# Performance work log

Measured on AMD Instinct MI355X. Metric: run time of the kernel, lower is better.

## Reference

```python
import jax, jax.numpy as jnp
import numpy as np

D_MODEL = 2048
NUM_Q_HEADS = 32
NUM_KV_HEADS = 8
HEAD_DIM = D_MODEL // NUM_Q_HEADS  # 64
NUM_GROUPS = NUM_Q_HEADS // NUM_KV_HEADS  # 4


def setup_inputs() -> dict:
    key = jax.random.key(0)
    ks = jax.random.split(key, 9)
    s = 1.0 / np.sqrt(D_MODEL)
    x = jax.random.normal(ks[0], (2, 2048, D_MODEL), dtype=jnp.float32)
    Wq = jax.random.uniform(ks[1], (D_MODEL, NUM_Q_HEADS * HEAD_DIM), jnp.float32, -s, s)
    bq = jax.random.uniform(ks[2], (NUM_Q_HEADS * HEAD_DIM,), jnp.float32, -s, s)
    Wk = jax.random.uniform(ks[3], (D_MODEL, NUM_KV_HEADS * HEAD_DIM), jnp.float32, -s, s)
    bk = jax.random.uniform(ks[4], (NUM_KV_HEADS * HEAD_DIM,), jnp.float32, -s, s)
    Wv = jax.random.uniform(ks[5], (D_MODEL, NUM_KV_HEADS * HEAD_DIM), jnp.float32, -s, s)
    bv = jax.random.uniform(ks[6], (NUM_KV_HEADS * HEAD_DIM,), jnp.float32, -s, s)
    Wo = jax.random.uniform(ks[7], (D_MODEL, D_MODEL), jnp.float32, -s, s)
    bo = jax.random.uniform(ks[8], (D_MODEL,), jnp.float32, -s, s)
    return {"x": x, "Wq": Wq, "bq": bq, "Wk": Wk, "bk": bk,
            "Wv": Wv, "bv": bv, "Wo": Wo, "bo": bo}


def reference(x, Wq, bq, Wk, bk, Wv, bv, Wo, bo):
    B, T, C = x.shape
    Hkv, G, Dh = NUM_KV_HEADS, NUM_GROUPS, HEAD_DIM
    # projections
    q = (x @ Wq + bq).reshape(B, T, Hkv, G, Dh)   # group G query heads per kv head
    k = (x @ Wk + bk).reshape(B, T, Hkv, Dh)
    v = (x @ Wv + bv).reshape(B, T, Hkv, Dh)
    scale = 1.0 / np.sqrt(Dh).astype(np.float32)
    # scores: [B, Hkv, G, T, T] (kv head broadcast over its G query heads)
    scores = jnp.einsum('btkgd,bskd->bkgts', q, k) * scale
    attn = jax.nn.softmax(scores, axis=-1)
    out = jnp.einsum('bkgts,bskd->btkgd', attn, v).reshape(B, T, C)
    return out @ Wo + bo
```

## Files before the change

### kernel.cpp

```cpp
#include <hip/hip_runtime.h>
#include <cstdint>
#include <cstddef>
#include <math.h>

typedef uint16_t bf16;
typedef __attribute__((ext_vector_type(8))) __bf16 bf16x8;
typedef __attribute__((ext_vector_type(4))) float f32x4;
typedef __attribute__((ext_vector_type(16))) float f32x16;

#define MFMA16(a,b,c) __builtin_amdgcn_mfma_f32_16x16x32_bf16((a),(b),(c),0,0,0)
#define MFMA32(a,b,c) __builtin_amdgcn_mfma_f32_32x32x16_bf16((a),(b),(c),0,0,0)

__device__ __forceinline__ uint16_t f2bf(float f){
  uint32_t u = __float_as_uint(f);
  return (uint16_t)((u + 0x7fffu + ((u >> 16) & 1u)) >> 16);
}
__device__ __forceinline__ uint32_t pk2(float lo, float hi){
  return (uint32_t)f2bf(lo) | ((uint32_t)f2bf(hi) << 16);
}

__device__ __forceinline__ void gload_lds16(const void* g, void* l){
  __builtin_amdgcn_global_load_lds((const __attribute__((address_space(1))) void*)g,
                                   (__attribute__((address_space(3))) void*)l, 16, 0, 0);
}

__device__ __forceinline__ void transpose64(const float* __restrict__ in, bf16* __restrict__ out,
                                            int R, int C, int c0, int r0, float* tileRaw){
  float (*tile)[65] = reinterpret_cast<float(*)[65]>(tileRaw);
  int t = threadIdx.x;
  int fx = t & 15, fy = t >> 4;
  #pragma unroll
  for (int i = 0; i < 4; i++){
    int r = fy + i*16;
    float4 v = *reinterpret_cast<const float4*>(in + (size_t)(r0 + r)*C + c0 + fx*4);
    tile[r][fx*4+0] = v.x; tile[r][fx*4+1] = v.y;
    tile[r][fx*4+2] = v.z; tile[r][fx*4+3] = v.w;
  }
  __syncthreads();
  int gx = t & 7, gy = t >> 3;
  #pragma unroll
  for (int i = 0; i < 2; i++){
    int c = gy + i*32;
    int rr = gx*8;
    union { bf16 h[8]; uint4 u; } pk_;
    #pragma unroll
    for (int j = 0; j < 8; j++) pk_.h[j] = f2bf(tile[rr+j][c]);
    *reinterpret_cast<uint4*>(out + (size_t)(c0 + c)*R + r0 + rr) = pk_.u;
  }
}

__global__ void k_prep(const float* __restrict__ x, bf16* __restrict__ xb,
                       const float* __restrict__ Wq, bf16* __restrict__ WqT,
                       const float* __restrict__ Wk, bf16* __restrict__ WkT,
                       const float* __restrict__ Wv, bf16* __restrict__ WvT,
                       const float* __restrict__ Wo, bf16* __restrict__ WoT,
                       const float* __restrict__ bq, const float* __restrict__ bk,
                       const float* __restrict__ bv, float* __restrict__ biasAll){
  __shared__ __align__(16) float tile[64*65];
  int b = blockIdx.x;
  if (b < 8192){
    int i = (b * 256 + threadIdx.x) * 4;
    float4 v = *reinterpret_cast<const float4*>(x + i);
    uint2 pkv = make_uint2(pk2(v.x, v.y), pk2(v.z, v.w));
    *reinterpret_cast<uint2*>(xb + i) = pkv;
  } else if (b < 9216){
    int idx = b - 8192;
    transpose64(Wq, WqT, 2048, 2048, (idx & 31)*64, (idx >> 5)*64, tile);
  } else if (b < 9472){
    int idx = b - 9216;
    transpose64(Wk, WkT, 2048, 512, (idx & 7)*64, (idx >> 3)*64, tile);
  } else if (b < 9728){
    int idx = b - 9472;
    transpose64(Wv, WvT, 2048, 512, (idx & 7)*64, (idx >> 3)*64, tile);
  } else if (b < 10752){
    int idx = b - 9728;
    transpose64(Wo, WoT, 2048, 2048, (idx & 31)*64, (idx >> 5)*64, tile);
  } else {
    int j = (b - 10752)*1024 + threadIdx.x*4;
    float4 v;
    if (j < 2048)      v = *reinterpret_cast<const float4*>(bq + j);
    else if (j < 2560) v = *reinterpret_cast<const float4*>(bk + j - 2048);
    else               v = *reinterpret_cast<const float4*>(bv + j - 2560);
    *reinterpret_cast<float4*>(biasAll + j) = v;
  }
}

__device__ __forceinline__ void gemm256x192_core(
    const bf16* __restrict__ Abase, const bf16* __restrict__ Btbase,
    char* lds, f32x4 acc[8][3])
{
  const int tid = threadIdx.x;
  const int wid = tid >> 6, lane = tid & 63;
  const int wm = wid >> 2, wn = wid & 3;
  const int lr = lane & 15, lg = lane >> 4;
  const f32x4 vzero = {0.f, 0.f, 0.f, 0.f};
  #pragma unroll
  for (int m = 0; m < 8; m++)
    #pragma unroll
    for (int n = 0; n < 3; n++)
      acc[m][n] = vzero;

  int srcA[4], srcB[3];
  #pragma unroll
  for (int i = 0; i < 4; i++){
    int db = i*8192 + tid*16;
    int row = db >> 7, sp = (db >> 4) & 7, sl = sp ^ (row & 7);
    srcA[i] = row*2048 + sl*8;
  }
  #pragma unroll
  for (int i = 0; i < 3; i++){
    int db = i*8192 + tid*16;
    int row = db >> 7, sp = (db >> 4) & 7, sl = sp ^ (row & 7);
    srcB[i] = row*2048 + sl*8;
  }
  const int dOf = wid*1024;

  int ksl[2];
  #pragma unroll
  for (int ks = 0; ks < 2; ks++) ksl[ks] = (((ks*4 + lg) ^ (lr & 7)) << 4);
  const int aB = wm*16384 + lr*128;
  const int bB = wn*6144 + lr*128;

  #define STG_A(bufOff, koff) do { \
    gload_lds16(Abase + (koff) + srcA[0], lds + (bufOff) + dOf); \
    gload_lds16(Abase + (koff) + srcA[1], lds + (bufOff) + 8192 + dOf); \
    gload_lds16(Abase + (koff) + srcA[2], lds + (bufOff) + 16384 + dOf); \
    gload_lds16(Abase + (koff) + srcA[3], lds + (bufOff) + 24576 + dOf); \
  } while(0)
  #define STG_B(bufOff, koff) do { \
    gload_lds16(Btbase + (koff) + srcB[0], lds + (bufOff) + dOf); \
    gload_lds16(Btbase + (koff) + srcB[1], lds + (bufOff) + 8192 + dOf); \
    gload_lds16(Btbase + (koff) + srcB[2], lds + (bufOff) + 16384 + dOf); \
  } while(0)

  STG_B(98304, 0);
  STG_A(0, 0);
  STG_A(32768, 64);
  asm volatile("s_waitcnt vmcnt(4)" ::: "memory");
  __builtin_amdgcn_s_barrier();

  int aOff = 0;
  int bOff = 98304;
  for (int t = 0; t < 32; t++){
    const int aStg = (aOff == 0) ? 65536 : aOff - 32768;
    const int bNxt = bOff ^ 24576;

    if (t < 31) STG_B(bNxt, (t+1)*64);
    if (t < 30) STG_A(aStg, (t+2)*64);

    bf16x8 afr[8][2], bfr[3][2];
    #pragma unroll
    for (int am = 0; am < 8; am++)
      #pragma unroll
      for (int ks = 0; ks < 2; ks++)
        afr[am][ks] = *reinterpret_cast<const bf16x8*>(lds + aOff + aB + am*2048 + ksl[ks]);
    #pragma unroll
    for (int bn = 0; bn < 3; bn++)
      #pragma unroll
      for (int ks = 0; ks < 2; ks++)
        bfr[bn][ks] = *reinterpret_cast<const bf16x8*>(lds + bOff + bB + bn*2048 + ksl[ks]);

    __builtin_amdgcn_s_setprio(1);
    #pragma unroll
    for (int am = 0; am < 8; am++)
      #pragma unroll
      for (int bn = 0; bn < 3; bn++)
        #pragma unroll
        for (int ks = 0; ks < 2; ks++)
          acc[am][bn] = MFMA16(afr[am][ks], bfr[bn][ks], acc[am][bn]);
    __builtin_amdgcn_s_setprio(0);

    if (t < 30)       asm volatile("s_waitcnt vmcnt(4)" ::: "memory");
    else if (t == 30) asm volatile("s_waitcnt vmcnt(0)" ::: "memory");
    __builtin_amdgcn_s_barrier();

    aOff = (aOff == 65536) ? 0 : aOff + 32768;
    bOff = bNxt;
  }
  #undef STG_A
  #undef STG_B
}

__device__ __forceinline__ void gemm256x128_core(
    const bf16* __restrict__ Abase, const bf16* __restrict__ Btbase,
    char* lds, f32x4 acc[4][4])
{
  const int tid = threadIdx.x;
  const int wid = tid >> 6, lane = tid & 63;
  const int wm = wid >> 1, wn = wid & 1;
  const int lr = lane & 15, lg = lane >> 4;
  const f32x4 vzero = {0.f, 0.f, 0.f, 0.f};
  #pragma unroll
  for (int m = 0; m < 4; m++)
    #pragma unroll
    for (int n = 0; n < 4; n++)
      acc[m][n] = vzero;

  int srcA[4], srcB[2];
  #pragma unroll
  for (int i = 0; i < 4; i++){
    int db = i*8192 + tid*16;
    int row = db >> 7, sp = (db >> 4) & 7, sl = sp ^ (row & 7);
    srcA[i] = row*2048 + sl*8;
  }
  #pragma unroll
  for (int i = 0; i < 2; i++){
    int db = i*8192 + tid*16;
    int row = db >> 7, sp = (db >> 4) & 7, sl = sp ^ (row & 7);
    srcB[i] = row*2048 + sl*8;
  }
  const int dOf = wid*1024;

  int ksl[2];
  #pragma unroll
  for (int ks = 0; ks < 2; ks++) ksl[ks] = (((ks*4 + lg) ^ (lr & 7)) << 4);
  const int aB = wm*8192 + lr*128;
  const int bB = wn*8192 + lr*128;

  #define STG_A(bufOff, koff) do { \
    gload_lds16(Abase + (koff) + srcA[0], lds + (bufOff) + dOf); \
    gload_lds16(Abase + (koff) + srcA[1], lds + (bufOff) + 8192 + dOf); \
    gload_lds16(Abase + (koff) + srcA[2], lds + (bufOff) + 16384 + dOf); \
    gload_lds16(Abase + (koff) + srcA[3], lds + (bufOff) + 24576 + dOf); \
  } while(0)
  #define STG_B(bufOff, koff) do { \
    gload_lds16(Btbase + (koff) + srcB[0], lds + (bufOff) + dOf); \
    gload_lds16(Btbase + (koff) + srcB[1], lds + (bufOff) + 8192 + dOf); \
  } while(0)

  STG_B(98304, 0);
  STG_A(0, 0);
  STG_B(114688, 64);
  STG_A(32768, 64);
  asm volatile("s_waitcnt vmcnt(6)" ::: "memory");
  __builtin_amdgcn_s_barrier();

  int aOff = 0;
  int bIdx = 0;
  for (int t = 0; t < 32; t++){
    const int bOff = 98304 + bIdx*16384;
    const int aStg = (aOff == 0) ? 65536 : aOff - 32768;
    const int bStg = 98304 + ((bIdx == 0) ? 2 : bIdx - 1)*16384;

    if (t < 30){
      STG_B(bStg, (t+2)*64);
      STG_A(aStg, (t+2)*64);
    }

    bf16x8 afr[4][2], bfr[4][2];
    #pragma unroll
    for (int am = 0; am < 4; am++)
      #pragma unroll
      for (int ks = 0; ks < 2; ks++)
        afr[am][ks] = *reinterpret_cast<const bf16x8*>(lds + aOff + aB + am*2048 + ksl[ks]);
    #pragma unroll
    for (int bn = 0; bn < 4; bn++)
      #pragma unroll
      for (int ks = 0; ks < 2; ks++)
        bfr[bn][ks] = *reinterpret_cast<const bf16x8*>(lds + bOff + bB + bn*2048 + ksl[ks]);

    __builtin_amdgcn_s_setprio(1);
    #pragma unroll
    for (int am = 0; am < 4; am++)
      #pragma unroll
      for (int bn = 0; bn < 4; bn++)
        #pragma unroll
        for (int ks = 0; ks < 2; ks++)
          acc[am][bn] = MFMA16(afr[am][ks], bfr[bn][ks], acc[am][bn]);
    __builtin_amdgcn_s_setprio(0);

    if (t < 30)       asm volatile("s_waitcnt vmcnt(6)" ::: "memory");
    else if (t == 30) asm volatile("s_waitcnt vmcnt(0)" ::: "memory");
    __builtin_amdgcn_s_barrier();

    aOff = (aOff == 65536) ? 0 : aOff + 32768;
    bIdx = (bIdx == 2) ? 0 : bIdx + 1;
  }
  #undef STG_A
  #undef STG_B
}

__global__ __launch_bounds__(512, 1) void k_qkv(
    const bf16* __restrict__ xb, const bf16* __restrict__ WT,
    const float* __restrict__ biasAll,
    bf16* __restrict__ qo, bf16* __restrict__ ko, bf16* __restrict__ vtp)
{
  __shared__ __align__(16) char lds[147456];
  int m0 = blockIdx.x * 256;
  int y  = blockIdx.y;
  f32x4 acc[8][3];
  gemm256x192_core(xb + (size_t)m0*2048, WT + (size_t)y*192*2048, lds, acc);
  const int tid = threadIdx.x, wid = tid >> 6, lane = tid & 63;
  const int wm = wid >> 2, wn = wid & 3, lr = lane & 15, lg = lane >> 4;
  #pragma unroll
  for (int bn = 0; bn < 3; bn++){
    int fb = y*192 + wn*48 + bn*16;
    float bb = biasAll[fb + lr];
    if (fb < 2048){
      #pragma unroll
      for (int am = 0; am < 8; am++)
        #pragma unroll
        for (int r = 0; r < 4; r++){
          int row = m0 + wm*128 + am*16 + lg*4 + r;
          qo[(size_t)row*2048 + fb + lr] = f2bf((acc[am][bn][r] + bb) * 0.18033688011112042f);
        }
    } else if (fb < 2560){
      int c = fb - 2048 + lr;
      #pragma unroll
      for (int am = 0; am < 8; am++)
        #pragma unroll
        for (int r = 0; r < 4; r++){
          int row = m0 + wm*128 + am*16 + lg*4 + r;
          ko[(size_t)row*512 + c] = f2bf(acc[am][bn][r] + bb);
        }
    } else {
      int vcol = fb - 2560 + lr;
      #pragma unroll
      for (int am = 0; am < 8; am++){
        int row0 = m0 + wm*128 + am*16 + lg*4;
        int bi = row0 >> 11, tl = row0 & 2047;
        union { bf16 h[4]; uint2 u; } pk_;
        #pragma unroll
        for (int r = 0; r < 4; r++) pk_.h[r] = f2bf(acc[am][bn][r] + bb);
        *reinterpret_cast<uint2*>(vtp + ((size_t)bi*512 + vcol)*2048 + tl) = pk_.u;
      }
    }
  }
}

__global__ __launch_bounds__(512, 1) void k_oproj(
    const bf16* __restrict__ ab, const bf16* __restrict__ WoT,
    const float* __restrict__ bo, float* __restrict__ outp)
{
  __shared__ __align__(16) char lds[147456];
  int m0 = blockIdx.x * 256, n0 = blockIdx.y * 128;
  f32x4 acc[4][4];
  gemm256x128_core(ab + (size_t)m0*2048, WoT + (size_t)n0*2048, lds, acc);
  const int tid = threadIdx.x, wid = tid >> 6, lane = tid & 63;
  const int wm = wid >> 1, wn = wid & 1, lr = lane & 15, lg = lane >> 4;
  #pragma unroll
  for (int bn = 0; bn < 4; bn++){
    int col = n0 + wn*64 + bn*16 + lr;
    float bb = bo[col];
    #pragma unroll
    for (int am = 0; am < 4; am++)
      #pragma unroll
      for (int r = 0; r < 4; r++){
        int row = m0 + wm*64 + am*16 + lg*4 + r;
        outp[(size_t)row*2048 + col] = acc[am][bn][r] + bb;
      }
  }
}

__global__ __launch_bounds__(512, 2) void k_flash(
    const bf16* __restrict__ q, const bf16* __restrict__ kmat,
    const bf16* __restrict__ vt, bf16* __restrict__ ao)
{
  __shared__ __align__(16) char lds[98304];
  const int tid = threadIdx.x;
  const int wid = tid >> 6, lane = tid & 63;
  const int l31 = lane & 31, hi = lane >> 5;
  const int bh = blockIdx.y;
  const int b = bh >> 5, hq = bh & 31, kvh = hq >> 2;
  const int qt = blockIdx.x;
  const int qrow0 = b*2048 + qt*512 + wid*64;

  bf16x8 qf[2][4];
  #pragma unroll
  for (int g = 0; g < 2; g++){
    const bf16* qrow = q + (size_t)(qrow0 + g*32 + l31)*2048 + hq*64 + hi*8;
    #pragma unroll
    for (int t = 0; t < 4; t++)
      qf[g][t] = *reinterpret_cast<const bf16x8*>(qrow + t*16);
  }

  f32x16 oacc[2][2];
  #pragma unroll
  for (int g = 0; g < 2; g++)
    #pragma unroll
    for (int n = 0; n < 2; n++)
      #pragma unroll
      for (int r = 0; r < 16; r++) oacc[g][n][r] = 0.f;
  float rsg[2][2];
  rsg[0][0]=0.f; rsg[0][1]=0.f; rsg[1][0]=0.f; rsg[1][1]=0.f;
  const f32x16 zv = {0.f,0.f,0.f,0.f,0.f,0.f,0.f,0.f,0.f,0.f,0.f,0.f,0.f,0.f,0.f,0.f};

  const int r7 = l31 & 7;
  int A[4];
  #pragma unroll
  for (int j = 0; j < 4; j++)
    A[j] = l31*128 + (((2*j + hi) ^ r7) << 4);

  const bf16* kbase = kmat + (size_t)b*2048*512 + kvh*64;
  const bf16* vbase = vt + ((size_t)b*512 + kvh*64)*2048;

  int kSrc[2], vSrc[2];
  const int dOf = wid*1024;
  #pragma unroll
  for (int i = 0; i < 2; i++){
    int kdb = i*8192 + tid*16;
    int krow = kdb >> 7, ksp = (kdb >> 4) & 7, ksl = ksp ^ (krow & 7);
    kSrc[i] = krow*512 + ksl*8;
    int o = tid*16;
    int vrow = o >> 7, vsp = (o >> 4) & 7, vsl = vsp ^ (vrow & 7);
    vSrc[i] = vrow*2048 + i*64 + vsl*8;
  }

  #define STAGE(bo, st_) do { \
    const bf16* kb_ = kbase + (size_t)(st_)*128*512; \
    const bf16* vb_ = vbase + (st_)*128; \
    gload_lds16(kb_ + kSrc[0], lds + (bo) + dOf); \
    gload_lds16(kb_ + kSrc[1], lds + (bo) + 8192 + dOf); \
    gload_lds16(vb_ + vSrc[0], lds + 49152 + (bo) + dOf); \
    gload_lds16(vb_ + vSrc[1], lds + 49152 + (bo) + 8192 + dOf); \
  } while(0)

  #define LDK(j, imm) (*reinterpret_cast<const bf16x8*>(lds + kOff + A[j] + (imm)))
  #define LDV(j, imm) (*reinterpret_cast<const bf16x8*>(lds + 49152 + kOff + A[j] + (imm)))

  STAGE(0, 0);
  STAGE(16384, 1);

  int kOff = 0;
  int sOff = 32768;
  for (int st = 0; st < 16; st++){
    if (st == 15) asm volatile("s_waitcnt vmcnt(0)" ::: "memory");
    else          asm volatile("s_waitcnt vmcnt(4)" ::: "memory");
    __builtin_amdgcn_sched_barrier(0);
    __builtin_amdgcn_s_barrier();
    __builtin_amdgcn_sched_barrier(0);
    if (st < 14){
      STAGE(sOff, st+2);
      sOff = (sOff == 32768) ? 0 : sOff + 16384;
    }

    #pragma unroll
    for (int c = 0; c < 2; c++){
      f32x16 sc[2][2];
      __builtin_amdgcn_s_setprio(1);
      #pragma unroll
      for (int t = 0; t < 4; t++){
        bf16x8 af0 = LDK(t, c*8192);
        bf16x8 af1 = LDK(t, c*8192 + 4096);
        if (t == 0){
          sc[0][0] = MFMA32(af0, qf[0][0], zv);
          sc[1][0] = MFMA32(af0, qf[1][0], zv);
          sc[0][1] = MFMA32(af1, qf[0][0], zv);
          sc[1][1] = MFMA32(af1, qf[1][0], zv);
        } else {
          sc[0][0] = MFMA32(af0, qf[0][t], sc[0][0]);
          sc[1][0] = MFMA32(af0, qf[1][t], sc[1][0]);
          sc[0][1] = MFMA32(af1, qf[0][t], sc[0][1]);
          sc[1][1] = MFMA32(af1, qf[1][t], sc[1][1]);
        }
      }
      __builtin_amdgcn_s_setprio(0);

      uint32_t pw[2][2][8];
      #pragma unroll
      for (int g = 0; g < 2; g++){
        #pragma unroll
        for (int n = 0; n < 2; n++)
          #pragma unroll
          for (int j = 0; j < 8; j++){
            float plo = __builtin_amdgcn_exp2f(sc[g][n][2*j]);
            float phi = __builtin_amdgcn_exp2f(sc[g][n][2*j+1]);
            rsg[g][j & 1] += plo + phi;
            asm("v_cvt_pk_bf16_f32 %0, %1, %2" : "=v"(pw[g][n][j]) : "v"(plo), "v"(phi));
          }
        #pragma unroll
        for (int n = 0; n < 2; n++)
          #pragma unroll
          for (int h = 0; h < 2; h++){
            asm volatile("v_permlane32_swap_b32 %0, %1" : "+v"(pw[g][n][h*4+0]), "+v"(pw[g][n][h*4+2]));
            asm volatile("v_permlane32_swap_b32 %0, %1" : "+v"(pw[g][n][h*4+1]), "+v"(pw[g][n][h*4+3]));
          }
      }

      __builtin_amdgcn_s_setprio(1);
      #pragma unroll
      for (int kk = 0; kk < 4; kk++){
        int n = kk >> 1, h = kk & 1;
        union { uint32_t w[4]; bf16x8 v; } pa0, pa1;
        #pragma unroll
        for (int w_ = 0; w_ < 4; w_++){ pa0.w[w_] = pw[0][n][h*4+w_]; pa1.w[w_] = pw[1][n][h*4+w_]; }
        #pragma unroll
        for (int nd = 0; nd < 2; nd++){
          bf16x8 vf = LDV(kk, c*8192 + nd*4096);
          oacc[0][nd] = MFMA32(pa0.v, vf, oacc[0][nd]);
          oacc[1][nd] = MFMA32(pa1.v, vf, oacc[1][nd]);
        }
      }
      __builtin_amdgcn_s_setprio(0);
    }
    kOff = (kOff == 32768) ? 0 : kOff + 16384;
  }
  #undef STAGE
  #undef LDK
  #undef LDV

  #pragma unroll
  for (int g = 0; g < 2; g++){
    float rs = rsg[g][0] + rsg[g][1];
    float l = rs + __shfl_xor(rs, 32);
    float linv = 1.f / l;
    float lv[16];
    #pragma unroll
    for (int r = 0; r < 16; r++){
      int qi = (r & 3) + 8*(r >> 2) + 4*hi;
      lv[r] = __shfl(linv, qi);
    }
    #pragma unroll
    for (int nd = 0; nd < 2; nd++)
      #pragma unroll
      for (int r = 0; r < 16; r++){
        int qi = (r & 3) + 8*(r >> 2) + 4*hi;
        int row = qrow0 + g*32 + qi;
        ao[(size_t)row*2048 + hq*64 + nd*32 + l31] = f2bf(oacc[g][nd][r] * lv[r]);
      }
  }
}

extern "C" void kernel_launch(void* const* d_in, const int* in_sizes, int n_in,
                              void* d_out, int out_size, void* d_ws, size_t ws_size,
                              hipStream_t stream)
{
  const float* x  = (const float*)d_in[0];
  const float* Wq = (const float*)d_in[1];
  const float* bq = (const float*)d_in[2];
  const float* Wk = (const float*)d_in[3];
  const float* bk = (const float*)d_in[4];
  const float* Wv = (const float*)d_in[5];
  const float* bv = (const float*)d_in[6];
  const float* Wo = (const float*)d_in[7];
  const float* bo = (const float*)d_in[8];
  float* out = (float*)d_out;

  char* ws = (char*)d_ws;
  size_t off = 0;
  auto alloc = [&](size_t bytes){ char* p = ws + off; off += (bytes + 255) & ~(size_t)255; return p; };
  bf16* xb  = (bf16*)alloc(2*2048*2048*2);
  bf16* WqT = (bf16*)alloc(2048*2048*2);
  bf16* WkT = (bf16*)alloc(512*2048*2);
  bf16* WvT = (bf16*)alloc(512*2048*2);
  bf16* WoT = (bf16*)alloc(2048*2048*2);
  bf16* qb  = (bf16*)alloc(4096*2048*2);
  bf16* kb  = (bf16*)alloc((size_t)4096*512*2);
  bf16* vtb = (bf16*)alloc((size_t)4096*512*2);
  float* biasAll = (float*)alloc(3072*4);
  bf16* aob = xb;

  k_prep<<<10755, 256, 0, stream>>>(x, xb, Wq, WqT, Wk, WkT, Wv, WvT, Wo, WoT, bq, bk, bv, biasAll);
  k_qkv<<<dim3(16,16), 512, 0, stream>>>(xb, WqT, biasAll, qb, kb, vtb);
  k_flash<<<dim3(4,64), 512, 0, stream>>>(qb, kb, vtb, aob);
  k_oproj<<<dim3(16,16), 512, 0, stream>>>(aob, WoT, bo, out);
}
```

Before: 179.1 us.

## Drop LDS staging in flash attention; read K/V fragments directly from global

The flash-attention kernel no longer stages K and V tiles into shared memory with async global-to-LDS loads and barriers. Each wave now loads its K and V MFMA fragments straight from global memory, relying on L1/L2 caching. Blocks shrink to 256 threads covering 256 query rows with a doubled grid, and the launch bounds now target three blocks per CU. This removes LDS traffic and barrier synchronisation, but each wave now fetches K/V on its own, which multiplies global/cache traffic and loses the software prefetch pipeline, so memory latency is exposed inside the MFMA loop.

```diff
diff --git a/kernel.cpp b/kernel.cpp
--- a/kernel.cpp
+++ b/kernel.cpp
@@ -352,18 +352,17 @@
   }
 }
 
-__global__ __launch_bounds__(512, 2) void k_flash(
+__global__ __launch_bounds__(256, 3) void k_flash(
     const bf16* __restrict__ q, const bf16* __restrict__ kmat,
     const bf16* __restrict__ vt, bf16* __restrict__ ao)
 {
-  __shared__ __align__(16) char lds[98304];
   const int tid = threadIdx.x;
   const int wid = tid >> 6, lane = tid & 63;
   const int l31 = lane & 31, hi = lane >> 5;
   const int bh = blockIdx.y;
   const int b = bh >> 5, hq = bh & 31, kvh = hq >> 2;
   const int qt = blockIdx.x;
-  const int qrow0 = b*2048 + qt*512 + wid*64;
+  const int qrow0 = b*2048 + qt*256 + wid*64;
 
   bf16x8 qf[2][4];
   #pragma unroll
@@ -385,119 +384,70 @@
   rsg[0][0]=0.f; rsg[0][1]=0.f; rsg[1][0]=0.f; rsg[1][1]=0.f;
   const f32x16 zv = {0.f,0.f,0.f,0.f,0.f,0.f,0.f,0.f,0.f,0.f,0.f,0.f,0.f,0.f,0.f,0.f};
 
-  const int r7 = l31 & 7;
-  int A[4];
-  #pragma unroll
-  for (int j = 0; j < 4; j++)
-    A[j] = l31*128 + (((2*j + hi) ^ r7) << 4);
-
-  const bf16* kbase = kmat + (size_t)b*2048*512 + kvh*64;
-  const bf16* vbase = vt + ((size_t)b*512 + kvh*64)*2048;
-
-  int kSrc[2], vSrc[2];
-  const int dOf = wid*1024;
-  #pragma unroll
-  for (int i = 0; i < 2; i++){
-    int kdb = i*8192 + tid*16;
-    int krow = kdb >> 7, ksp = (kdb >> 4) & 7, ksl = ksp ^ (krow & 7);
-    kSrc[i] = krow*512 + ksl*8;
-    int o = tid*16;
-    int vrow = o >> 7, vsp = (o >> 4) & 7, vsl = vsp ^ (vrow & 7);
-    vSrc[i] = vrow*2048 + i*64 + vsl*8;
-  }
-
-  #define STAGE(bo, st_) do { \
-    const bf16* kb_ = kbase + (size_t)(st_)*128*512; \
-    const bf16* vb_ = vbase + (st_)*128; \
-    gload_lds16(kb_ + kSrc[0], lds + (bo) + dOf); \
-    gload_lds16(kb_ + kSrc[1], lds + (bo) + 8192 + dOf); \
-    gload_lds16(vb_ + vSrc[0], lds + 49152 + (bo) + dOf); \
-    gload_lds16(vb_ + vSrc[1], lds + 49152 + (bo) + 8192 + dOf); \
-  } while(0)
-
-  #define LDK(j, imm) (*reinterpret_cast<const bf16x8*>(lds + kOff + A[j] + (imm)))
-  #define LDV(j, imm) (*reinterpret_cast<const bf16x8*>(lds + 49152 + kOff + A[j] + (imm)))
-
-  STAGE(0, 0);
-  STAGE(16384, 1);
-
-  int kOff = 0;
-  int sOff = 32768;
-  for (int st = 0; st < 16; st++){
-    if (st == 15) asm volatile("s_waitcnt vmcnt(0)" ::: "memory");
-    else          asm volatile("s_waitcnt vmcnt(4)" ::: "memory");
-    __builtin_amdgcn_sched_barrier(0);
-    __builtin_amdgcn_s_barrier();
-    __builtin_amdgcn_sched_barrier(0);
-    if (st < 14){
-      STAGE(sOff, st+2);
-      sOff = (sOff == 32768) ? 0 : sOff + 16384;
+  const bf16* k0 = kmat + ((size_t)b*2048 + l31)*512 + kvh*64 + hi*8;
+  const bf16* k1 = k0 + 32*512;
+  const bf16* v0 = vt + ((size_t)b*512 + kvh*64 + l31)*2048 + hi*8;
+  const bf16* v1 = v0 + (size_t)32*2048;
+
+  for (int st = 0; st < 32; st++){
+    f32x16 sc[2][2];
+    #pragma unroll
+    for (int t = 0; t < 4; t++){
+      bf16x8 af0 = *reinterpret_cast<const bf16x8*>(k0 + t*16);
+      bf16x8 af1 = *reinterpret_cast<const bf16x8*>(k1 + t*16);
+      if (t == 0){
+        sc[0][0] = MFMA32(af0, qf[0][0], zv);
+        sc[1][0] = MFMA32(af0, qf[1][0], zv);
+        sc[0][1] = MFMA32(af1, qf[0][0], zv);
+        sc[1][1] = MFMA32(af1, qf[1][0], zv);
+      } else {
+        sc[0][0] = MFMA32(af0, qf[0][t], sc[0][0]);
+        sc[1][0] = MFMA32(af0, qf[1][t], sc[1][0]);
+        sc[0][1] = MFMA32(af1, qf[0][t], sc[0][1]);
+        sc[1][1] = MFMA32(af1, qf[1][t], sc[1][1]);
+      }
     }
 
-    #pragma unroll
-    for (int c = 0; c < 2; c++){
-      f32x16 sc[2][2];
-      __builtin_amdgcn_s_setprio(1);
-      #pragma unroll
-      for (int t = 0; t < 4; t++){
-        bf16x8 af0 = LDK(t, c*8192);
-        bf16x8 af1 = LDK(t, c*8192 + 4096);
-        if (t == 0){
-          sc[0][0] = MFMA32(af0, qf[0][0], zv);
-          sc[1][0] = MFMA32(af0, qf[1][0], zv);
-          sc[0][1] = MFMA32(af1, qf[0][0], zv);
-          sc[1][1] = MFMA32(af1, qf[1][0], zv);
-        } else {
-          sc[0][0] = MFMA32(af0, qf[0][t], sc[0][0]);
-          sc[1][0] = MFMA32(af0, qf[1][t], sc[1][0]);
-          sc[0][1] = MFMA32(af1, qf[0][t], sc[0][1]);
-          sc[1][1] = MFMA32(af1, qf[1][t], sc[1][1]);
+    uint32_t pw[2][2][8];
+    #pragma unroll
+    for (int g = 0; g < 2; g++){
+      #pragma unroll
+      for (int n = 0; n < 2; n++)
+        #pragma unroll
+        for (int j = 0; j < 8; j++){
+          float plo = __builtin_amdgcn_exp2f(sc[g][n][2*j]);
+          float phi = __builtin_amdgcn_exp2f(sc[g][n][2*j+1]);
+          rsg[g][j & 1] += plo + phi;
+          asm("v_cvt_pk_bf16_f32 %0, %1, %2" : "=v"(pw[g][n][j]) : "v"(plo), "v"(phi));
         }
+      #pragma unroll
+      for (int n = 0; n < 2; n++)
+        #pragma unroll
+        for (int h = 0; h < 2; h++){
+          asm volatile("v_permlane32_swap_b32 %0, %1" : "+v"(pw[g][n][h*4+0]), "+v"(pw[g][n][h*4+2]));
+          asm volatile("v_permlane32_swap_b32 %0, %1" : "+v"(pw[g][n][h*4+1]), "+v"(pw[g][n][h*4+3]));
+        }
+    }
+
+    #pragma unroll
+    for (int kk = 0; kk < 4; kk++){
+      int n = kk >> 1, h = kk & 1;
+      union { uint32_t w[4]; bf16x8 v; } pa0, pa1;
+      #pragma unroll
+      for (int w_ = 0; w_ < 4; w_++){ pa0.w[w_] = pw[0][n][h*4+w_]; pa1.w[w_] = pw[1][n][h*4+w_]; }
+      {
+        bf16x8 vf0 = *reinterpret_cast<const bf16x8*>(v0 + kk*16);
+        bf16x8 vf1 = *reinterpret_cast<const bf16x8*>(v1 + kk*16);
+        oacc[0][0] = MFMA32(pa0.v, vf0, oacc[0][0]);
+        oacc[1][0] = MFMA32(pa1.v, vf0, oacc[1][0]);
+        oacc[0][1] = MFMA32(pa0.v, vf1, oacc[0][1]);
+        oacc[1][1] = MFMA32(pa1.v, vf1, oacc[1][1]);
       }
-      __builtin_amdgcn_s_setprio(0);
-
-      uint32_t pw[2][2][8];
-      #pragma unroll
-      for (int g = 0; g < 2; g++){
-        #pragma unroll
-        for (int n = 0; n < 2; n++)
-          #pragma unroll
-          for (int j = 0; j < 8; j++){
-            float plo = __builtin_amdgcn_exp2f(sc[g][n][2*j]);
-            float phi = __builtin_amdgcn_exp2f(sc[g][n][2*j+1]);
-            rsg[g][j & 1] += plo + phi;
-            asm("v_cvt_pk_bf16_f32 %0, %1, %2" : "=v"(pw[g][n][j]) : "v"(plo), "v"(phi));
-          }
-        #pragma unroll
-        for (int n = 0; n < 2; n++)
-          #pragma unroll
-          for (int h = 0; h < 2; h++){
-            asm volatile("v_permlane32_swap_b32 %0, %1" : "+v"(pw[g][n][h*4+0]), "+v"(pw[g][n][h*4+2]));
-            asm volatile("v_permlane32_swap_b32 %0, %1" : "+v"(pw[g][n][h*4+1]), "+v"(pw[g][n][h*4+3]));
-          }
-      }
-
-      __builtin_amdgcn_s_setprio(1);
-      #pragma unroll
-      for (int kk = 0; kk < 4; kk++){
-        int n = kk >> 1, h = kk & 1;
-        union { uint32_t w[4]; bf16x8 v; } pa0, pa1;
-        #pragma unroll
-        for (int w_ = 0; w_ < 4; w_++){ pa0.w[w_] = pw[0][n][h*4+w_]; pa1.w[w_] = pw[1][n][h*4+w_]; }
-        #pragma unroll
-        for (int nd = 0; nd < 2; nd++){
-          bf16x8 vf = LDV(kk, c*8192 + nd*4096);
-          oacc[0][nd] = MFMA32(pa0.v, vf, oacc[0][nd]);
-          oacc[1][nd] = MFMA32(pa1.v, vf, oacc[1][nd]);
-        }
-      }
-      __builtin_amdgcn_s_setprio(0);
     }
-    kOff = (kOff == 32768) ? 0 : kOff + 16384;
-  }
-  #undef STAGE
-  #undef LDK
-  #undef LDV
+
+    k0 += 64*512; k1 += 64*512;
+    v0 += 64;     v1 += 64;
+  }
 
   #pragma unroll
   for (int g = 0; g < 2; g++){
@@ -552,6 +502,6 @@
 
   k_prep<<<10755, 256, 0, stream>>>(x, xb, Wq, WqT, Wk, WkT, Wv, WvT, Wo, WoT, bq, bk, bv, biasAll);
   k_qkv<<<dim3(16,16), 512, 0, stream>>>(xb, WqT, biasAll, qb, kb, vtb);
-  k_flash<<<dim3(4,64), 512, 0, stream>>>(qb, kb, vtb, aob);
+  k_flash<<<dim3(8,64), 256, 0, stream>>>(qb, kb, vtb, aob);
   k_oproj<<<dim3(16,16), 512, 0, stream>>>(aob, WoT, bo, out);
 }
```

After: 266.9 us. 49.0% more time.
